# Kernel optimization log

Hardware: AMD Instinct MI355X
Metric: run time of the kernel (lower is better)

## Reference

```python
import jax, jax.numpy as jnp
import numpy as np

NT, NC, E = 50, 20, 64   # n_types, n_categories, embedding_size
B, L = 4, 256            # batch, seq_len
TIME_SCALE = 100.0


def setup_inputs() -> dict:
    key = jax.random.key(0)
    ks = jax.random.split(key, 12)
    times = jnp.sort(jax.random.uniform(ks[0], (B, L), dtype=jnp.float32) * TIME_SCALE, axis=1)
    types = jax.random.randint(ks[1], (B, L), 0, NT)
    cats = jax.random.randint(ks[2], (B, L), 0, NC)
    p = lambda k, s: 0.1 * jax.random.normal(k, s, dtype=jnp.float32)
    # type_emb / a positively biased so intensity stays > 0 (log is taken on it)
    type_emb = 0.05 * jax.random.normal(ks[3], (NT, E), dtype=jnp.float32) + 0.1
    a = 0.1 * jnp.abs(jax.random.normal(ks[5], (NT, E), dtype=jnp.float32)) + 0.2
    return {
        "event_times": times,
        "event_types": types,
        "event_categories": cats,
        "T": 128,
        "type_emb": type_emb,
        "cat_emb": p(ks[4], (NC, E)),
        "a": a,
        "b": p(ks[6], (NC, E)),
        "A": p(ks[7], (NT, NT, E)),
        "P": p(ks[8], (NT, NT, E)),
        "Bm": p(ks[9], (NC, NC, E)),
        "Q": p(ks[10], (NC, NC, E)),
    }


def _intensity(type_emb, cat_emb, a, b, A, P, Bm, Q, times, types, cats, hist_len, t_now):
    """Intensity over all event types given history times[:hist_len]. Returns [NT]."""
    Lr = times.shape[0]
    mask = jnp.arange(Lr) < hist_len                       # [L]
    td = jnp.where(mask, t_now - times, 0.0)               # [L]
    # --- type channel: m[t,e] = sum_s f[t]*A[k_s,t]*exp(-f[t]*P[k_s,t]*f[k_s]*td_s)*f[k_s]
    f_eth = type_emb[types]                                # [L,E]
    decay = jnp.exp(-(type_emb[None] * P[types]) * f_eth[:, None, :] * td[:, None, None])  # [L,NT,E]
    contrib = type_emb[None] * A[types] * decay * f_eth[:, None, :]
    m = jnp.sum(jnp.where(mask[:, None, None], contrib, 0.0), axis=0)   # [NT,E]
    # --- category channel: n[c,e] analogous with g/B/Q
    g_eth = cat_emb[cats]                                  # [L,E]
    cdecay = jnp.exp(-(cat_emb[None] * Q[cats]) * g_eth[:, None, :] * td[:, None, None])  # [L,NC,E]
    ccontrib = cat_emb[None] * Bm[cats] * cdecay * g_eth[:, None, :]
    n = jnp.sum(jnp.where(mask[:, None, None], ccontrib, 0.0), axis=0)  # [NC,E]
    last_cat = cats[jnp.maximum(hist_len - 1, 0)]          # cats[-1] of the history
    base = type_emb * a                                    # [NT,E]
    full = jnp.sum(base + type_emb * b[last_cat][None] + m + type_emb * n[last_cat][None], axis=1)
    empty = jnp.sum(jax.nn.softplus(base), axis=1)         # empty-history branch
    return jnp.where(hist_len == 0, empty, full)           # [NT]


def reference(event_times, event_types, event_categories, T, type_emb, cat_emb, a, b, A, P, Bm, Q):
    Tf = jnp.float32(T)
    Lr = event_times.shape[1]
    inten = lambda ts, ty, ct, h, tn: _intensity(type_emb, cat_emb, a, b, A, P, Bm, Q, ts, ty, ct, h, tn)

    def per_seq(times, types, cats):
        def step(ll, i):
            lam_vec = inten(times, types, cats, i, times[i])
            lam = lam_vec[types[i]]
            c = jnp.where(times[i] >= 0, jnp.log(lam + 1e-16) + lam, 0.0)
            return ll + c, None
        ll, _ = jax.lax.scan(step, jnp.float32(0.0), jnp.arange(Lr))
        total_int = inten(times, types, cats, Lr, Tf)       # intensity at horizon T, full history
        I0 = jnp.sum(jax.nn.softplus(type_emb * a))         # empty-history intensity summed over types
        integral = jnp.sum(total_int) * (Tf - times[-1]) + I0 * times[0]
        return ll, integral

    lls, ints = jax.vmap(per_seq)(event_times, event_types, event_categories)
    return -(jnp.sum(lls) - jnp.sum(ints))
```

## Files before the change

### kernel.cpp

```cpp
#include <hip/hip_runtime.h>

#define NTY 50
#define NCA 20
#define ED  64
#define NB  4
#define SL  256

#define TYPE_BLOCKS (NB * NTY)
#define CAT_BLOCKS  (NB * NCA)
#define MAIN_BLOCKS (TYPE_BLOCKS + CAT_BLOCKS)
#define NTHREADS 512
#define NWAVES   (NTHREADS / 64)
#define JTILE    16

#define WS_M  0
#define WS_N  (NB * SL)
#define WS_IT (2 * NB * SL)
#define WS_NT (2 * NB * SL + NB * NTY)

__device__ __forceinline__ float softplusf(float x) {
    return (x > 0.f) ? x + log1pf(__expf(-x)) : log1pf(__expf(x));
}

__device__ __forceinline__ float waveReduceSum(float v) {
    #pragma unroll
    for (int off = 32; off > 0; off >>= 1) v += __shfl_down(v, off, 64);
    return v;
}

struct SharedBuf {
    float times_sh[SL + 1];
    int   types_sh[SL];
    int   cats_sh[SL];
    int   kcnt[NTY];
    int   csr_off[NTY + 1];
    int   csr_pos[SL];
    int   evl[SL];
    int   evcnt;
    float trA;
    float trB[NCA];
    float qmat[JTILE][NTHREADS];
    float nmat[NCA][ED];
    float temb[NTY][ED];
};

template <bool IS_TYPE, int NK, int EPT>
__device__ __forceinline__ void run_channel(
        int b, int tgt, int tid,
        const float* __restrict__ times, const int* __restrict__ types,
        const int* __restrict__ cats, float Tf,
        const float* __restrict__ type_emb, const float* __restrict__ cat_emb,
        const float* __restrict__ amat, const float* __restrict__ bmat,
        const float* __restrict__ Cmat, const float* __restrict__ Pmat,
        float* __restrict__ ws, SharedBuf& sh) {
    const int lane = tid & 63;
    const int w    = tid >> 6;
    constexpr int GPK  = ED / EPT;
    constexpr int NACT = NK * GPK;
    const int myk  = tid / GPK;
    const int e0   = (tid % GPK) * EPT;
    const bool active = tid < NACT;
    const int base = b * SL;

    float Rr[EPT], Cr[EPT], W[EPT];
    if (active) {
        #pragma unroll
        for (int m = 0; m < EPT; ++m) {
            const int e = e0 + m;
            const float tr = IS_TYPE ? type_emb[tgt * ED + e] : cat_emb[tgt * ED + e];
            const float f  = IS_TYPE ? type_emb[myk * ED + e] : cat_emb[myk * ED + e];
            Cr[m] = tr * Cmat[(myk * NK + tgt) * ED + e] * f;
            Rr[m] = tr * Pmat[(myk * NK + tgt) * ED + e] * f;
            W[m]  = 0.f;
        }
    }
    float trE = 0.f, aE = 0.f;
    if (IS_TYPE) {
        trE = type_emb[tgt * ED + lane];
        aE  = amat[tgt * ED + lane];
    }

    if (tid < SL) {
        sh.times_sh[tid] = times[base + tid];
        sh.types_sh[tid] = types[base + tid];
        sh.cats_sh[tid]  = cats[base + tid];
    }
    if (tid == 0) sh.times_sh[SL] = Tf;
    if (!IS_TYPE) {
        for (int idx = tid; idx < NTY * ED; idx += NTHREADS)
            (&sh.temb[0][0])[idx] = type_emb[idx];
    }
    __syncthreads();

    const int* keys = IS_TYPE ? sh.types_sh : sh.cats_sh;

    for (int k = w; k < NK; k += NWAVES) {
        int cnt = 0;
        #pragma unroll
        for (int c = 0; c < SL / 64; ++c)
            cnt += __popcll(__ballot(keys[lane + 64 * c] == k));
        if (lane == 0) sh.kcnt[k] = cnt;
    }
    if (w == NWAVES - 1) {
        int run = 0;
        #pragma unroll
        for (int c = 0; c < SL / 64; ++c) {
            const int p = lane + 64 * c;
            const bool pred = (p >= 1) && (IS_TYPE ? (sh.types_sh[p] == tgt)
                                                   : (sh.cats_sh[p - 1] == tgt));
            const unsigned long long mk = __ballot(pred);
            if (pred) sh.evl[run + __popcll(mk & ((1ull << lane) - 1ull))] = p;
            run += __popcll(mk);
        }
        if (lane == 0) sh.evcnt = run;
    }
    __syncthreads();

    if (w == 0) {
        int v = (lane < NK) ? sh.kcnt[lane] : 0;
        #pragma unroll
        for (int off = 1; off < 64; off <<= 1) {
            const int u = __shfl_up(v, off, 64);
            if (lane >= off) v += u;
        }
        if (lane < NK) sh.csr_off[lane + 1] = v;
        if (lane == 0) sh.csr_off[0] = 0;
    }
    if (IS_TYPE) {
        if (w == 1) {
            const float r = waveReduceSum(trE * aE);
            if (lane == 0) sh.trA = r;
        }
        for (int c = w; c < NCA; c += NWAVES) {
            const float r = waveReduceSum(trE * bmat[c * ED + lane]);
            if (lane == 0) sh.trB[c] = r;
        }
    }
    __syncthreads();

    for (int k = w; k < NK; k += NWAVES) {
        int bp = sh.csr_off[k];
        #pragma unroll
        for (int c = 0; c < SL / 64; ++c) {
            const int p = lane + 64 * c;
            const bool pred = (keys[p] == k);
            const unsigned long long mk = __ballot(pred);
            if (pred) sh.csr_pos[bp + __popcll(mk & ((1ull << lane) - 1ull))] = p;
            bp += __popcll(mk);
        }
    }
    __syncthreads();

    const int ne    = sh.evcnt;
    const int lastc = sh.cats_sh[SL - 1];
    int       m     = active ? sh.csr_off[myk] : 0;
    const int mend  = active ? sh.csr_off[myk + 1] : 0;

    for (int j0 = 0; j0 <= ne; j0 += JTILE) {
        const int jhi = min(j0 + JTILE - 1, ne);

        if (active) {
            for (int j = j0; j <= jhi; ++j) {
                const int ie = (j < ne) ? sh.evl[j] : SL;
                while (m < mend) {
                    const int pos = sh.csr_pos[m];
                    if (pos >= ie) break;
                    const float ts = sh.times_sh[pos];
                    #pragma unroll
                    for (int mm = 0; mm < EPT; ++mm) W[mm] += __expf(Rr[mm] * ts);
                    ++m;
                }
                const float tau = sh.times_sh[ie];
                if (IS_TYPE || j < ne) {
                    float q = 0.f;
                    #pragma unroll
                    for (int mm = 0; mm < EPT; ++mm) {
                        float v = Cr[mm] * __expf(-Rr[mm] * tau) * W[mm];
                        if (!IS_TYPE) v *= sh.temb[sh.types_sh[ie]][e0 + mm];
                        q += v;
                    }
                    sh.qmat[j - j0][tid] = q;
                } else {
                    #pragma unroll
                    for (int mm = 0; mm < EPT; ++mm)
                        sh.nmat[myk][e0 + mm] = Cr[mm] * __expf(-Rr[mm] * tau) * W[mm];
                }
            }
        }
        __syncthreads();

        for (int jj = w; jj <= jhi - j0; jj += NWAVES) {
            const int j = j0 + jj;
            if (!IS_TYPE && j == ne) continue;
            const int ie = (j < ne) ? sh.evl[j] : SL;
            float p = 0.f;
            #pragma unroll
            for (int m2 = 0; m2 < NWAVES; ++m2) {
                const int src = lane + 64 * m2;
                if (src < NACT) p += sh.qmat[jj][src];
            }
            const float r = waveReduceSum(p);
            if (lane == 0) {
                if (IS_TYPE) {
                    if (j < ne) ws[WS_M + b * SL + ie] = r + sh.trA + sh.trB[sh.cats_sh[ie - 1]];
                    else        ws[WS_IT + b * NTY + tgt] = r + sh.trA;
                } else {
                    ws[WS_N + b * SL + ie] = r;
                }
            }
        }
        __syncthreads();
    }

    if (!IS_TYPE && tgt == lastc && w == 0) {
        float nacc = 0.f;
        #pragma unroll
        for (int k = 0; k < NCA; ++k) nacc += sh.nmat[k][lane];
        ws[WS_NT + b * ED + lane] = nacc;
    }
}

__global__ __launch_bounds__(NTHREADS) void hawkes_main(
        const float* __restrict__ times,
        const int*   __restrict__ types,
        const int*   __restrict__ cats,
        const int*   __restrict__ Tp,
        const float* __restrict__ type_emb,
        const float* __restrict__ cat_emb,
        const float* __restrict__ amat,
        const float* __restrict__ bmat,
        const float* __restrict__ A,
        const float* __restrict__ P,
        const float* __restrict__ Bm,
        const float* __restrict__ Q,
        float* __restrict__ ws) {
    const int blk = blockIdx.x;
    const int tid = threadIdx.x;
    __shared__ SharedBuf sh;

    const float Tf = (float)Tp[0];

    if (blk < TYPE_BLOCKS) {
        const int b = blk / NTY, tgt = blk % NTY;
        run_channel<true, NTY, 8>(b, tgt, tid, times, types, cats, Tf,
                                  type_emb, cat_emb, amat, bmat, A, P, ws, sh);
    } else {
        const int cb = blk - TYPE_BLOCKS;
        const int b = cb / NCA, tgt = cb % NCA;
        run_channel<false, NCA, 4>(b, tgt, tid, times, types, cats, Tf,
                                   type_emb, cat_emb, amat, bmat, Bm, Q, ws, sh);
    }
}

__global__ __launch_bounds__(256) void hawkes_final(
        const float* __restrict__ times,
        const int*   __restrict__ types,
        const int*   __restrict__ cats,
        const int*   __restrict__ Tp,
        const float* __restrict__ type_emb,
        const float* __restrict__ amat,
        const float* __restrict__ bmat,
        const float* __restrict__ ws,
        float* __restrict__ out) {
    const int tid  = threadIdx.x;
    const int lane = tid & 63;
    const int w    = tid >> 6;

    __shared__ float tsl[4][ED];
    __shared__ float wred[4], i0red[4], intb[4];

    const float Tf = (float)Tp[0];

    float llp = 0.f;
    const int i = tid + 1;
    if (i < SL) {
        #pragma unroll
        for (int bb = 0; bb < NB; ++bb) {
            const float lam = ws[WS_M + bb * SL + i] + ws[WS_N + bb * SL + i];
            llp += logf(lam + 1e-16f) + lam;
        }
    }

    const int t0 = types[w * SL];
    const float v0 = softplusf(type_emb[t0 * ED + lane] * amat[t0 * ED + lane]);

    float tsp = 0.f, i0p = 0.f;
    for (int t = w; t < NTY; t += 4) {
        const float tv = type_emb[t * ED + lane];
        tsp += tv;
        i0p += softplusf(tv * amat[t * ED + lane]);
    }
    tsl[w][lane] = tsp;

    const float lam0 = waveReduceSum(v0);
    const float wll  = waveReduceSum(llp);
    const float wi0  = waveReduceSum(i0p);
    if (lane == 0) {
        wred[w]  = wll + logf(lam0 + 1e-16f) + lam0;
        i0red[w] = wi0;
    }
    __syncthreads();

    const float TS_l = tsl[0][lane] + tsl[1][lane] + tsl[2][lane] + tsl[3][lane];
    const int   lc   = cats[w * SL + SL - 1];
    const float bbv  = bmat[lc * ED + lane] + ws[WS_NT + w * ED + lane];
    const float its  = (lane < NTY) ? ws[WS_IT + w * NTY + lane] : 0.f;
    const float ip   = waveReduceSum(its + bbv * TS_l);
    if (lane == 0) intb[w] = ip * (Tf - times[w * SL + SL - 1]);
    __syncthreads();

    if (tid == 0) {
        const float ll = wred[0] + wred[1] + wred[2] + wred[3];
        const float I0 = i0red[0] + i0red[1] + i0red[2] + i0red[3];
        const float t0s = times[0] + times[SL] + times[2 * SL] + times[3 * SL];
        const float tot = intb[0] + intb[1] + intb[2] + intb[3] + I0 * t0s;
        out[0] = -(ll - tot);
    }
}

extern "C" void kernel_launch(void* const* d_in, const int* in_sizes, int n_in,
                              void* d_out, int out_size, void* d_ws, size_t ws_size,
                              hipStream_t stream) {
    const float* times    = (const float*)d_in[0];
    const int*   types    = (const int*)  d_in[1];
    const int*   cats     = (const int*)  d_in[2];
    const int*   Tp       = (const int*)  d_in[3];
    const float* type_emb = (const float*)d_in[4];
    const float* cat_emb  = (const float*)d_in[5];
    const float* amat     = (const float*)d_in[6];
    const float* bmat     = (const float*)d_in[7];
    const float* A        = (const float*)d_in[8];
    const float* P        = (const float*)d_in[9];
    const float* Bm       = (const float*)d_in[10];
    const float* Q        = (const float*)d_in[11];
    float* out = (float*)d_out;
    float* ws  = (float*)d_ws;

    hawkes_main<<<MAIN_BLOCKS, NTHREADS, 0, stream>>>(times, types, cats, Tp,
                                                      type_emb, cat_emb, amat, bmat,
                                                      A, P, Bm, Q, ws);
    hawkes_final<<<1, 256, 0, stream>>>(times, types, cats, Tp,
                                        type_emb, amat, bmat, ws, out);
}
```

Before: 109.3 us.

## Fuse final reduction into main kernel via last-block counter and retune tiling

Removes the separate final kernel launch: each main block increments a global counter after its writes, and the last block to finish runs the log-likelihood and integral reduction. Also halves the j-tile to 8 with an unrolled event prefetch, packs times with CSR positions into a float2 array, drops the shared type-embedding copy in favour of direct global reads, and adds a launch-bounds occupancy hint. This trades a kernel launch for a memset plus atomics and a serialized tail in one block, and relies on atomic-read ordering being correct.

Measured after the change: 109.5 us. Within noise of the previous version (+0.1%).

```diff
diff --git a/kernel.cpp b/kernel.cpp
--- a/kernel.cpp
+++ b/kernel.cpp
@@ -11,12 +11,13 @@
 #define MAIN_BLOCKS (TYPE_BLOCKS + CAT_BLOCKS)
 #define NTHREADS 512
 #define NWAVES   (NTHREADS / 64)
-#define JTILE    16
-
-#define WS_M  0
-#define WS_N  (NB * SL)
-#define WS_IT (2 * NB * SL)
-#define WS_NT (2 * NB * SL + NB * NTY)
+#define JTILE    8
+
+#define WS_M   0
+#define WS_N   (NB * SL)
+#define WS_IT  (2 * NB * SL)
+#define WS_NT  (2 * NB * SL + NB * NTY)
+#define WS_CNT (WS_NT + NB * ED)
 
 __device__ __forceinline__ float softplusf(float x) {
     return (x > 0.f) ? x + log1pf(__expf(-x)) : log1pf(__expf(x));
@@ -29,19 +30,21 @@
 }
 
 struct SharedBuf {
-    float times_sh[SL + 1];
-    int   types_sh[SL];
-    int   cats_sh[SL];
-    int   kcnt[NTY];
-    int   csr_off[NTY + 1];
-    int   csr_pos[SL];
-    int   evl[SL];
-    int   evcnt;
-    float trA;
-    float trB[NCA];
-    float qmat[JTILE][NTHREADS];
-    float nmat[NCA][ED];
-    float temb[NTY][ED];
+    float2 csr_td[SL];
+    float  times_sh[SL + 1];
+    int    types_sh[SL];
+    int    cats_sh[SL];
+    int    kcnt[NTY];
+    int    csr_off[NTY + 1];
+    int    evl[SL];
+    int    evcnt;
+    int    finflag;
+    float  trA;
+    float  trB[NCA];
+    float  qmat[JTILE][NTHREADS];
+    float  nmat[NCA][ED];
+    float  ftsl[4][ED];
+    float  fred[4], fi0[4], fintb[4];
 };
 
 template <bool IS_TYPE, int NK, int EPT>
@@ -83,13 +86,10 @@
     if (tid < SL) {
         sh.times_sh[tid] = times[base + tid];
         sh.types_sh[tid] = types[base + tid];
-        sh.cats_sh[tid]  = cats[base + tid];
+    } else {
+        sh.cats_sh[tid - SL] = cats[base + tid - SL];
     }
     if (tid == 0) sh.times_sh[SL] = Tf;
-    if (!IS_TYPE) {
-        for (int idx = tid; idx < NTY * ED; idx += NTHREADS)
-            (&sh.temb[0][0])[idx] = type_emb[idx];
-    }
     __syncthreads();
 
     const int* keys = IS_TYPE ? sh.types_sh : sh.cats_sh;
@@ -143,43 +143,60 @@
         #pragma unroll
         for (int c = 0; c < SL / 64; ++c) {
             const int p = lane + 64 * c;
-            const bool pred = (keys[p] == k);
-            const unsigned long long mk = __ballot(pred);
-            if (pred) sh.csr_pos[bp + __popcll(mk & ((1ull << lane) - 1ull))] = p;
+            const bool pr = (keys[p] == k);
+            const unsigned long long mk = __ballot(pr);
+            if (pr) {
+                const int d = bp + __popcll(mk & ((1ull << lane) - 1ull));
+                sh.csr_td[d] = make_float2(sh.times_sh[p], __int_as_float(p));
+            }
             bp += __popcll(mk);
         }
     }
     __syncthreads();
 
-    const int ne    = sh.evcnt;
-    const int lastc = sh.cats_sh[SL - 1];
-    int       m     = active ? sh.csr_off[myk] : 0;
-    const int mend  = active ? sh.csr_off[myk + 1] : 0;
+    const int ne   = sh.evcnt;
+    int       m    = active ? sh.csr_off[myk] : 0;
+    const int mend = active ? sh.csr_off[myk + 1] : 0;
 
     for (int j0 = 0; j0 <= ne; j0 += JTILE) {
         const int jhi = min(j0 + JTILE - 1, ne);
 
         if (active) {
-            for (int j = j0; j <= jhi; ++j) {
+            int iev[JTILE]; float tev[JTILE]; int tEv[JTILE];
+            #pragma unroll
+            for (int u = 0; u < JTILE; ++u) {
+                const int j = j0 + u;
                 const int ie = (j < ne) ? sh.evl[j] : SL;
+                iev[u] = ie;
+                tev[u] = sh.times_sh[ie];
+            }
+            if (!IS_TYPE) {
+                #pragma unroll
+                for (int u = 0; u < JTILE; ++u)
+                    tEv[u] = (j0 + u < ne) ? sh.types_sh[iev[u]] : 0;
+            }
+            #pragma unroll
+            for (int u = 0; u < JTILE; ++u) {
+                const int j = j0 + u;
+                if (j > ne) break;
+                const int   ie  = iev[u];
+                const float tau = tev[u];
                 while (m < mend) {
-                    const int pos = sh.csr_pos[m];
-                    if (pos >= ie) break;
-                    const float ts = sh.times_sh[pos];
+                    const float2 v = sh.csr_td[m];
+                    if (__float_as_int(v.y) >= ie) break;
                     #pragma unroll
-                    for (int mm = 0; mm < EPT; ++mm) W[mm] += __expf(Rr[mm] * ts);
+                    for (int mm = 0; mm < EPT; ++mm) W[mm] += __expf(Rr[mm] * v.x);
                     ++m;
                 }
-                const float tau = sh.times_sh[ie];
                 if (IS_TYPE || j < ne) {
                     float q = 0.f;
                     #pragma unroll
                     for (int mm = 0; mm < EPT; ++mm) {
-                        float v = Cr[mm] * __expf(-Rr[mm] * tau) * W[mm];
-                        if (!IS_TYPE) v *= sh.temb[sh.types_sh[ie]][e0 + mm];
-                        q += v;
+                        float t1 = Cr[mm] * __expf(-Rr[mm] * tau) * W[mm];
+                        if (!IS_TYPE) t1 *= type_emb[tEv[u] * ED + e0 + mm];
+                        q += t1;
                     }
-                    sh.qmat[j - j0][tid] = q;
+                    sh.qmat[u][tid] = q;
                 } else {
                     #pragma unroll
                     for (int mm = 0; mm < EPT; ++mm)
@@ -189,38 +206,41 @@
         }
         __syncthreads();
 
-        for (int jj = w; jj <= jhi - j0; jj += NWAVES) {
+        {
+            const int jj = w;
             const int j = j0 + jj;
-            if (!IS_TYPE && j == ne) continue;
-            const int ie = (j < ne) ? sh.evl[j] : SL;
-            float p = 0.f;
-            #pragma unroll
-            for (int m2 = 0; m2 < NWAVES; ++m2) {
-                const int src = lane + 64 * m2;
-                if (src < NACT) p += sh.qmat[jj][src];
-            }
-            const float r = waveReduceSum(p);
-            if (lane == 0) {
-                if (IS_TYPE) {
-                    if (j < ne) ws[WS_M + b * SL + ie] = r + sh.trA + sh.trB[sh.cats_sh[ie - 1]];
-                    else        ws[WS_IT + b * NTY + tgt] = r + sh.trA;
-                } else {
-                    ws[WS_N + b * SL + ie] = r;
+            if (jj <= jhi - j0 && !(!IS_TYPE && j == ne)) {
+                const int ie = (j < ne) ? sh.evl[j] : SL;
+                float p = 0.f;
+                #pragma unroll
+                for (int m2 = 0; m2 < NWAVES; ++m2) {
+                    const int src = lane + 64 * m2;
+                    if (src < NACT) p += sh.qmat[jj][src];
                 }
+                const float r = waveReduceSum(p);
+                if (lane == 0) {
+                    if (IS_TYPE) {
+                        if (j < ne) atomicExch(&ws[WS_M + b * SL + ie],
+                                               r + sh.trA + sh.trB[sh.cats_sh[ie - 1]]);
+                        else        atomicExch(&ws[WS_IT + b * NTY + tgt], r + sh.trA);
+                    } else {
+                        atomicExch(&ws[WS_N + b * SL + ie], r);
+                    }
+                }
             }
         }
         __syncthreads();
     }
 
-    if (!IS_TYPE && tgt == lastc && w == 0) {
+    if (!IS_TYPE && tgt == sh.cats_sh[SL - 1] && w == 0) {
         float nacc = 0.f;
         #pragma unroll
         for (int k = 0; k < NCA; ++k) nacc += sh.nmat[k][lane];
-        ws[WS_NT + b * ED + lane] = nacc;
-    }
-}
-
-__global__ __launch_bounds__(NTHREADS) void hawkes_main(
+        atomicExch(&ws[WS_NT + b * ED + lane], nacc);
+    }
+}
+
+__global__ __launch_bounds__(NTHREADS, 4) void hawkes_main(
         const float* __restrict__ times,
         const int*   __restrict__ types,
         const int*   __restrict__ cats,
@@ -233,7 +253,8 @@
         const float* __restrict__ P,
         const float* __restrict__ Bm,
         const float* __restrict__ Q,
-        float* __restrict__ ws) {
+        float* __restrict__ ws,
+        float* __restrict__ out) {
     const int blk = blockIdx.x;
     const int tid = threadIdx.x;
     __shared__ SharedBuf sh;
@@ -250,71 +271,73 @@
         run_channel<false, NCA, 4>(b, tgt, tid, times, types, cats, Tf,
                                    type_emb, cat_emb, amat, bmat, Bm, Q, ws, sh);
     }
-}
-
-__global__ __launch_bounds__(256) void hawkes_final(
-        const float* __restrict__ times,
-        const int*   __restrict__ types,
-        const int*   __restrict__ cats,
-        const int*   __restrict__ Tp,
-        const float* __restrict__ type_emb,
-        const float* __restrict__ amat,
-        const float* __restrict__ bmat,
-        const float* __restrict__ ws,
-        float* __restrict__ out) {
-    const int tid  = threadIdx.x;
-    const int lane = tid & 63;
-    const int w    = tid >> 6;
-
-    __shared__ float tsl[4][ED];
-    __shared__ float wred[4], i0red[4], intb[4];
-
-    const float Tf = (float)Tp[0];
-
-    float llp = 0.f;
-    const int i = tid + 1;
-    if (i < SL) {
-        #pragma unroll
-        for (int bb = 0; bb < NB; ++bb) {
-            const float lam = ws[WS_M + bb * SL + i] + ws[WS_N + bb * SL + i];
-            llp += logf(lam + 1e-16f) + lam;
-        }
-    }
-
-    const int t0 = types[w * SL];
-    const float v0 = softplusf(type_emb[t0 * ED + lane] * amat[t0 * ED + lane]);
-
-    float tsp = 0.f, i0p = 0.f;
-    for (int t = w; t < NTY; t += 4) {
-        const float tv = type_emb[t * ED + lane];
-        tsp += tv;
-        i0p += softplusf(tv * amat[t * ED + lane]);
-    }
-    tsl[w][lane] = tsp;
-
-    const float lam0 = waveReduceSum(v0);
-    const float wll  = waveReduceSum(llp);
-    const float wi0  = waveReduceSum(i0p);
-    if (lane == 0) {
-        wred[w]  = wll + logf(lam0 + 1e-16f) + lam0;
-        i0red[w] = wi0;
-    }
-    __syncthreads();
-
-    const float TS_l = tsl[0][lane] + tsl[1][lane] + tsl[2][lane] + tsl[3][lane];
-    const int   lc   = cats[w * SL + SL - 1];
-    const float bbv  = bmat[lc * ED + lane] + ws[WS_NT + w * ED + lane];
-    const float its  = (lane < NTY) ? ws[WS_IT + w * NTY + lane] : 0.f;
-    const float ip   = waveReduceSum(its + bbv * TS_l);
-    if (lane == 0) intb[w] = ip * (Tf - times[w * SL + SL - 1]);
-    __syncthreads();
-
+
+    __syncthreads();
     if (tid == 0) {
-        const float ll = wred[0] + wred[1] + wred[2] + wred[3];
-        const float I0 = i0red[0] + i0red[1] + i0red[2] + i0red[3];
-        const float t0s = times[0] + times[SL] + times[2 * SL] + times[3 * SL];
-        const float tot = intb[0] + intb[1] + intb[2] + intb[3] + I0 * t0s;
-        out[0] = -(ll - tot);
+        sh.finflag = 0;
+        __asm__ __volatile__("s_waitcnt vmcnt(0)" ::: "memory");
+        const unsigned old = atomicAdd((unsigned int*)&ws[WS_CNT], 1u);
+        if (old == MAIN_BLOCKS - 1u) sh.finflag = 1;
+    }
+    __syncthreads();
+    if (!sh.finflag) return;
+
+    {
+        const int lane = tid & 63;
+        const int w    = tid >> 6;
+        const int w4   = w & 3;
+
+        float llp = 0.f;
+        if (tid < SL - 1) {
+            const int i = tid + 1;
+            #pragma unroll
+            for (int bb = 0; bb < NB; ++bb) {
+                const float lam = atomicAdd(&ws[WS_M + bb * SL + i], 0.f)
+                                + atomicAdd(&ws[WS_N + bb * SL + i], 0.f);
+                llp += logf(lam + 1e-16f) + lam;
+            }
+        }
+
+        float tsp = 0.f, i0p = 0.f, v0 = 0.f;
+        if (w < 4) {
+            for (int t = w4; t < NTY; t += 4) {
+                const float tv = type_emb[t * ED + lane];
+                tsp += tv;
+                i0p += softplusf(tv * amat[t * ED + lane]);
+            }
+            sh.ftsl[w4][lane] = tsp;
+            const int t0 = types[w4 * SL];
+            v0 = softplusf(type_emb[t0 * ED + lane] * amat[t0 * ED + lane]);
+        }
+        const float wll  = waveReduceSum(llp);
+        const float lam0 = waveReduceSum(v0);
+        const float wi0  = waveReduceSum(i0p);
+        if (w < 4 && lane == 0) {
+            sh.fred[w4] = wll + logf(lam0 + 1e-16f) + lam0;
+            sh.fi0[w4]  = wi0;
+        }
+        __syncthreads();
+
+        if (w < 4) {
+            const float TS_l = sh.ftsl[0][lane] + sh.ftsl[1][lane]
+                             + sh.ftsl[2][lane] + sh.ftsl[3][lane];
+            const int   lc  = cats[w4 * SL + SL - 1];
+            const float bbv = bmat[lc * ED + lane]
+                            + atomicAdd(&ws[WS_NT + w4 * ED + lane], 0.f);
+            const float its = (lane < NTY) ? atomicAdd(&ws[WS_IT + w4 * NTY + lane], 0.f) : 0.f;
+            const float ip  = waveReduceSum(its + bbv * TS_l);
+            if (lane == 0) sh.fintb[w4] = ip * (Tf - times[w4 * SL + SL - 1]);
+        }
+        __syncthreads();
+
+        if (tid == 0) {
+            const float ll  = sh.fred[0] + sh.fred[1] + sh.fred[2] + sh.fred[3];
+            const float I0  = sh.fi0[0] + sh.fi0[1] + sh.fi0[2] + sh.fi0[3];
+            const float t0s = times[0] + times[SL] + times[2 * SL] + times[3 * SL];
+            const float tot = sh.fintb[0] + sh.fintb[1] + sh.fintb[2] + sh.fintb[3]
+                            + I0 * t0s;
+            out[0] = -(ll - tot);
+        }
     }
 }
 
@@ -336,9 +359,9 @@
     float* out = (float*)d_out;
     float* ws  = (float*)d_ws;
 
+    hipMemsetAsync(ws + WS_CNT, 0, sizeof(unsigned int), stream);
+
     hawkes_main<<<MAIN_BLOCKS, NTHREADS, 0, stream>>>(times, types, cats, Tp,
                                                       type_emb, cat_emb, amat, bmat,
-                                                      A, P, Bm, Q, ws);
-    hawkes_final<<<1, 256, 0, stream>>>(times, types, cats, Tp,
-                                        type_emb, amat, bmat, ws, out);
-}
+                                                      A, P, Bm, Q, ws, out);
+}
```
